# Optimization experiments

Hardware: AMD Instinct MI355X
Metric: run time of the kernel (lower is better)

The kernel has to match this reference:

```python
import jax, jax.numpy as jnp
import numpy as np
import math

B, C, N, M = 4, 128, 4096, 4096

def setup_inputs() -> dict:
    key = jax.random.key(0)
    ks = jax.random.split(key, 8)
    return {
        "x1": jax.random.normal(ks[0], (B, C, N), dtype=jnp.float32),
        "p1": jax.random.normal(ks[1], (B, 3, N), dtype=jnp.float32),
        "x2": jax.random.normal(ks[2], (B, C, M), dtype=jnp.float32),
        "p2": jax.random.normal(ks[3], (B, 3, M), dtype=jnp.float32),
        "Wq": jax.random.normal(ks[4], (C, C), dtype=jnp.float32) * 0.05,
        "Wk": jax.random.normal(ks[5], (C, C), dtype=jnp.float32) * 0.05,
        "Wv": jax.random.normal(ks[6], (C, C), dtype=jnp.float32) * 0.05,
        "Wpos": jax.random.normal(ks[7], (C, 3), dtype=jnp.float32) * 0.05,
    }

def reference(x1, p1, x2, p2, Wq, Wk, Wv, Wpos):
    # Conv1d with kernel_size=1, no bias == per-point matmul over channel dim.
    # NOTE: original forward uses self.pos for BOTH p1 and p2 (pos1 conv unused).
    pos = jnp.einsum('ck,bkn->bcn', Wpos, p1)   # [B,C,N]
    pos1 = jnp.einsum('ck,bkm->bcm', Wpos, p2)  # [B,C,M]
    q = jnp.einsum('dc,bcn->bdn', Wq, x1 + pos)   # [B,C,N]
    k = jnp.einsum('dc,bcm->bdm', Wk, x2 + pos1)  # [B,C,M]
    v = jnp.einsum('dc,bcm->bdm', Wv, x2)         # [B,C,M]
    scale = math.sqrt(q.shape[1])  # sqrt(C) -- q.shape[-2] in (B,C,N) layout
    energy = jnp.einsum('bcn,bcm->bnm', q, k) / scale  # [B,N,M]
    attention = jax.nn.softmax(energy, axis=-1)
    vout = jnp.einsum('bnm,bcm->bnc', attention, v)    # [B,N,C]
    out = jnp.swapaxes(vout, 1, 2) + x1                # [B,C,N] residual
    return jnp.swapaxes(out, 1, 2)                     # [B,N,C]
```

## Files before the change

kernel.cpp:

```cpp
#include <hip/hip_runtime.h>
#include <hip/hip_bf16.h>

#define B_ 4
#define C_ 128
#define N_ 4096
#define M_ 4096

typedef __bf16 bf16;
typedef __bf16 bf16x8 __attribute__((ext_vector_type(8)));
typedef float f32x4 __attribute__((ext_vector_type(4)));
typedef float f32x16 __attribute__((ext_vector_type(16)));

#define MFMA16(a, b, c) __builtin_amdgcn_mfma_f32_16x16x32_bf16(a, b, c, 0, 0, 0)
#define MFMA32(a, b, c) __builtin_amdgcn_mfma_f32_32x32x16_bf16(a, b, c, 0, 0, 0)

__device__ inline void gll16(const bf16* g, bf16* l) {
    __builtin_amdgcn_global_load_lds(
        (const __attribute__((address_space(1))) void*)g,
        (__attribute__((address_space(3))) void*)l, 16, 0, 0);
}

__device__ inline unsigned cvtpk(float a, float b) {
    unsigned r;
    asm("v_cvt_pk_bf16_f32 %0, %1, %2" : "=v"(r) : "v"(a), "v"(b));
    return r;
}

__global__ __launch_bounds__(256) void wcvt_kernel(
    const float* __restrict__ Wq, const float* __restrict__ Wk,
    const float* __restrict__ Wv, bf16* __restrict__ Wb) {
    int i = (blockIdx.x * 256 + threadIdx.x) * 4;
    const float* src = (i < 16384) ? Wq : (i < 32768) ? Wk : Wv;
    int off = i & 16383;
    float4 v = *(const float4*)(src + off);
    union { ushort4 u4; bf16 h[4]; } pk;
    pk.h[0] = (bf16)v.x; pk.h[1] = (bf16)v.y;
    pk.h[2] = (bf16)v.z; pk.h[3] = (bf16)v.w;
    *(ushort4*)(Wb + i) = pk.u4;
}

__global__ __launch_bounds__(512) void kvproj_kernel(
    const float* __restrict__ x2, const float* __restrict__ p2,
    const bf16* __restrict__ Wb, const float* __restrict__ Wpos,
    bf16* __restrict__ Kt, bf16* __restrict__ Vt) {
    __shared__ __align__(16) bf16 xp2[64 * 136];
    __shared__ __align__(16) bf16 xr2[64 * 136];
    __shared__ float pp[3 * 64], wls[384];

    const int t = threadIdx.x;
    const int b = blockIdx.y;
    const int n0 = blockIdx.x * 64;

    if (t < 48) {
        int k3 = t / 16, i4 = (t & 15) * 4;
        *(float4*)&pp[k3 * 64 + i4] =
            *(const float4*)(p2 + ((size_t)b * 3 + k3) * N_ + n0 + i4);
    } else if (t < 144) {
        int i4 = (t - 48) * 4;
        *(float4*)&wls[i4] = *(const float4*)(Wpos + i4);
    }
    __syncthreads();

    #pragma unroll
    for (int k = 0; k < 4; ++k) {
        int s = t + k * 512;
        int c = s >> 4, n4 = (s & 15) * 4;
        float4 xv = *(const float4*)(x2 + ((size_t)b * C_ + c) * N_ + n0 + n4);
        float w0 = wls[c * 3 + 0], w1 = wls[c * 3 + 1], w2 = wls[c * 3 + 2];
        const float* xa = &xv.x;
        #pragma unroll
        for (int j = 0; j < 4; ++j) {
            float pos = w0 * pp[n4 + j] + w1 * pp[64 + n4 + j] + w2 * pp[128 + n4 + j];
            xp2[(n4 + j) * 136 + c] = (bf16)(xa[j] + pos);
            xr2[(n4 + j) * 136 + c] = (bf16)xa[j];
        }
    }
    __syncthreads();

    const int w = t >> 6;
    const int lane = t & 63;
    const int col = lane & 15, quad = lane >> 4;
    const int band = w & 3;
    const int nl = band * 16 + col;
    const bool isK = (w < 4);

    const bf16* src = isK ? xp2 : xr2;
    const bf16* Wm = Wb + (isK ? 16384 : 32768);

    bf16x8 bx[4];
    #pragma unroll
    for (int cs = 0; cs < 4; ++cs)
        bx[cs] = *(const bf16x8*)&src[nl * 136 + cs * 32 + quad * 8];

    if (isK) {
        #pragma unroll
        for (int dt = 0; dt < 8; ++dt) {
            f32x4 acc = {0.f, 0.f, 0.f, 0.f};
            #pragma unroll
            for (int cs = 0; cs < 4; ++cs) {
                bf16x8 wf = *(const bf16x8*)(Wm + (dt * 16 + col) * 128 + cs * 32 + quad * 8);
                acc = MFMA16(bx[cs], wf, acc);
            }
            #pragma unroll
            for (int r = 0; r < 4; ++r) {
                int n = n0 + band * 16 + quad * 4 + r;
                Kt[((size_t)b * N_ + n) * C_ + dt * 16 + col] = (bf16)acc[r];
            }
        }
    } else {
        #pragma unroll
        for (int dt = 0; dt < 8; ++dt) {
            f32x4 acc = {0.f, 0.f, 0.f, 0.f};
            #pragma unroll
            for (int cs = 0; cs < 4; ++cs) {
                bf16x8 wf = *(const bf16x8*)(Wm + (dt * 16 + col) * 128 + cs * 32 + quad * 8);
                acc = MFMA16(wf, bx[cs], acc);
            }
            #pragma unroll
            for (int r = 0; r < 4; ++r)
                Vt[((size_t)b * C_ + dt * 16 + quad * 4 + r) * (size_t)M_ + n0 + nl] = (bf16)acc[r];
        }
    }
}

__global__ __launch_bounds__(512) void attn_kernel(
    const bf16* __restrict__ Kt, const bf16* __restrict__ Vt,
    const float* __restrict__ x1, const float* __restrict__ p1,
    const bf16* __restrict__ Wb, const float* __restrict__ Wpos,
    float* __restrict__ out) {
    __shared__ __align__(16) char smem[132096];

    const int t = threadIdx.x;
    const int w = t >> 6;
    const int lane = t & 63;
    const int col = lane & 31;
    const int hi = lane >> 5;
    const int kg = w & 3;
    const int qg = w >> 2;

    const int g0 = blockIdx.x;
    const int xcd = g0 & 7;
    const int b = xcd >> 1;
    const int qt = (xcd & 1) + ((g0 >> 3) << 1);
    const int n0 = qt * 64;

    const float KS = 0.12752107168406815f;

    const bf16* Kbase = Kt + (size_t)b * M_ * C_;
    const bf16* Vbase = Vt + (size_t)b * C_ * M_;

    bf16* xq = (bf16*)smem;
    float* ppq = (float*)(smem + 17408);
    float* wlsq = (float*)(smem + 18176);

    if (t < 48) {
        int k3 = t / 16, i4 = (t & 15) * 4;
        *(float4*)&ppq[k3 * 64 + i4] =
            *(const float4*)(p1 + ((size_t)b * 3 + k3) * N_ + n0 + i4);
    } else if (t < 144) {
        int i4 = (t - 48) * 4;
        *(float4*)&wlsq[i4] = *(const float4*)(Wpos + i4);
    }
    __syncthreads();

    #pragma unroll
    for (int k = 0; k < 4; ++k) {
        int s = t + k * 512;
        int c = s >> 4, n4 = (s & 15) * 4;
        float4 xv = *(const float4*)(x1 + ((size_t)b * C_ + c) * N_ + n0 + n4);
        float w0 = wlsq[c * 3 + 0], w1 = wlsq[c * 3 + 1], w2 = wlsq[c * 3 + 2];
        const float* xa = &xv.x;
        #pragma unroll
        for (int j = 0; j < 4; ++j) {
            float pos = w0 * ppq[n4 + j] + w1 * ppq[64 + n4 + j] + w2 * ppq[128 + n4 + j];
            xq[(n4 + j) * 136 + c] = (bf16)(xa[j] + pos);
        }
    }
    __syncthreads();

    {
        const int colq = lane & 15, quadq = lane >> 4;
        const int nlq = (w & 3) * 16 + colq;
        bf16x8 bxq[4];
        #pragma unroll
        for (int cs = 0; cs < 4; ++cs)
            bxq[cs] = *(const bf16x8*)&xq[nlq * 136 + cs * 32 + quadq * 8];
        __syncthreads();
        const int dt0 = (w >> 2) * 4;
        #pragma unroll
        for (int di = 0; di < 4; ++di) {
            int dt = dt0 + di;
            f32x4 acc = {0.f, 0.f, 0.f, 0.f};
            #pragma unroll
            for (int cs = 0; cs < 4; ++cs) {
                bf16x8 wf = *(const bf16x8*)(Wb + (dt * 16 + colq) * 128 + cs * 32 + quadq * 8);
                acc = MFMA16(bxq[cs], wf, acc);
            }
            #pragma unroll
            for (int r = 0; r < 4; ++r)
                xq[((w & 3) * 16 + quadq * 4 + r) * 136 + dt * 16 + colq] = (bf16)acc[r];
        }
        __syncthreads();
    }

    bf16x8 qf[8];
    #pragma unroll
    for (int cs = 0; cs < 8; ++cs)
        qf[cs] = *(const bf16x8*)&xq[(qg * 32 + col) * 136 + cs * 16 + hi * 8];
    asm volatile("s_waitcnt lgkmcnt(0)" ::: "memory");
    __builtin_amdgcn_sched_barrier(0);
    __builtin_amdgcn_s_barrier();

    f32x16 oacc[4];
    #pragma unroll
    for (int i = 0; i < 4; ++i)
        #pragma unroll
        for (int j = 0; j < 16; ++j) oacc[i][j] = 0.f;
    float lacc = 0.f;

    const int key_l = (kg << 5) + col;
    const int kxor = (key_l & 15) << 4;

    const bf16* kpp[4];
    const bf16* vpp[4];
    #pragma unroll
    for (int i = 0; i < 4; ++i) {
        int g = ((w << 2) + i) * 64 + lane;
        int row = g >> 4;
        int sp = (g & 15) ^ (row & 15);
        kpp[i] = Kbase + (size_t)row * C_ + sp * 8;
        vpp[i] = Vbase + (size_t)row * M_ + sp * 8;
    }

    auto stageK = [&](char* dst) {
        #pragma unroll
        for (int i = 0; i < 4; ++i) {
            gll16(kpp[i], (bf16*)dst + ((w << 2) + i) * 512);
            kpp[i] += 128 * C_;
        }
    };
    auto stageV = [&](char* dst) {
        #pragma unroll
        for (int i = 0; i < 4; ++i) {
            gll16(vpp[i], (bf16*)dst + ((w << 2) + i) * 512);
            vpp[i] += 128;
        }
    };

    stageK(smem);
    stageV(smem + 65536);
    stageK(smem + 32768);

    f32x16 sA0, sA1, sB0, sB1;

    auto qkc = [&](const char* kbBuf, f32x16& T0, f32x16& T1) {
        #pragma unroll
        for (int q = 0; q < 16; ++q) { T0[q] = 0.f; T1[q] = 0.f; }
        const char* kbp = kbBuf + key_l * 256;
        __builtin_amdgcn_s_setprio(1);
        #pragma unroll
        for (int cs = 0; cs < 4; ++cs) {
            bf16x8 kf = *(const bf16x8*)(kbp + ((((cs << 1) + hi) << 4) ^ kxor));
            T0 = MFMA32(kf, qf[cs], T0);
        }
        #pragma unroll
        for (int cs = 4; cs < 8; ++cs) {
            bf16x8 kf = *(const bf16x8*)(kbp + ((((cs << 1) + hi) << 4) ^ kxor));
            T1 = MFMA32(kf, qf[cs], T1);
        }
        __builtin_amdgcn_s_setprio(0);
    };

    auto smpv = [&](f32x16& S0, f32x16& S1, const char* vbBuf) {
        float p[16];
        #pragma unroll
        for (int r = 0; r < 16; ++r) {
            float e = fminf((S0[r] + S1[r]) * KS, 60.f);
            p[r] = __builtin_amdgcn_exp2f(e);
        }
        {
            float s01 = (p[0] + p[1]) + (p[2] + p[3]);
            float s23 = (p[4] + p[5]) + (p[6] + p[7]);
            float s45 = (p[8] + p[9]) + (p[10] + p[11]);
            float s67 = (p[12] + p[13]) + (p[14] + p[15]);
            lacc += (s01 + s23) + (s45 + s67);
        }
        unsigned W0 = cvtpk(p[0], p[1]),  W1 = cvtpk(p[2], p[3]);
        unsigned W2 = cvtpk(p[4], p[5]),  W3 = cvtpk(p[6], p[7]);
        unsigned W4 = cvtpk(p[8], p[9]),  W5 = cvtpk(p[10], p[11]);
        unsigned W6 = cvtpk(p[12], p[13]), W7 = cvtpk(p[14], p[15]);
        unsigned X0 = hi ? W0 : W2, X1 = hi ? W1 : W3;
        unsigned Y0 = hi ? W4 : W6, Y1 = hi ? W5 : W7;
        X0 = __shfl_xor(X0, 32, 64);  X1 = __shfl_xor(X1, 32, 64);
        Y0 = __shfl_xor(Y0, 32, 64);  Y1 = __shfl_xor(Y1, 32, 64);
        uint4 u0, u1;
        u0.x = hi ? X0 : W0;  u0.y = hi ? X1 : W1;
        u0.z = hi ? W2 : X0;  u0.w = hi ? W3 : X1;
        u1.x = hi ? Y0 : W4;  u1.y = hi ? Y1 : W5;
        u1.z = hi ? W6 : Y0;  u1.w = hi ? W7 : Y1;
        bf16x8 af0 = __builtin_bit_cast(bf16x8, u0);
        bf16x8 af1 = __builtin_bit_cast(bf16x8, u1);

        __builtin_amdgcn_s_setprio(1);
        #pragma unroll
        for (int ct = 0; ct < 4; ++ct) {
            int c = (ct << 5) + col;
            const char* vbp = vbBuf + c * 256;
            int vxor = (c & 15) << 4;
            bf16x8 vf0 = *(const bf16x8*)(vbp + ((((kg << 2) + hi) << 4) ^ vxor));
            bf16x8 vf1 = *(const bf16x8*)(vbp + ((((kg << 2) + 2 + hi) << 4) ^ vxor));
            oacc[ct] = MFMA32(af0, vf0, oacc[ct]);
            oacc[ct] = MFMA32(af1, vf1, oacc[ct]);
        }
        __builtin_amdgcn_s_setprio(0);
    };

    asm volatile("s_waitcnt vmcnt(8)" ::: "memory");
    __builtin_amdgcn_sched_barrier(0);
    __builtin_amdgcn_s_barrier();
    __builtin_amdgcn_sched_barrier(0);
    qkc(smem, sA0, sA1);

    for (int jp = 0; jp < 16; ++jp) {
        const int j0 = jp * 2, j1 = j0 + 1;

        asm volatile("s_waitcnt vmcnt(0)" ::: "memory");
        __builtin_amdgcn_sched_barrier(0);
        __builtin_amdgcn_s_barrier();
        __builtin_amdgcn_sched_barrier(0);
        if (j0 < 31) stageV(smem + 98304);
        if (j0 < 30) stageK(smem);
        if (j0 < 31) qkc(smem + 32768, sB0, sB1);
        smpv(sA0, sA1, smem + 65536);
        asm volatile("s_waitcnt lgkmcnt(0)" ::: "memory");
        __builtin_amdgcn_sched_barrier(0);

        asm volatile("s_waitcnt vmcnt(0)" ::: "memory");
        __builtin_amdgcn_sched_barrier(0);
        __builtin_amdgcn_s_barrier();
        __builtin_amdgcn_sched_barrier(0);
        if (j1 < 31) stageV(smem + 65536);
        if (j1 < 30) stageK(smem + 32768);
        if (j1 < 31) qkc(smem, sA0, sA1);
        smpv(sB0, sB1, smem + 98304);
        asm volatile("s_waitcnt lgkmcnt(0)" ::: "memory");
        __builtin_amdgcn_sched_barrier(0);
    }

    __builtin_amdgcn_s_barrier();

    float* obuf = (float*)smem;
    float* lps  = (float*)(smem + 131072);

    lacc += __shfl_xor(lacc, 32, 64);
    if (hi == 0) lps[(kg << 6) + (qg << 5) + col] = lacc;

    #pragma unroll
    for (int ct = 0; ct < 4; ++ct)
        #pragma unroll
        for (int r = 0; r < 16; ++r) {
            int q = (r & 3) + ((r >> 2) << 3) + (hi << 2);
            obuf[kg * 8192 + ((qg << 5) + q) * 128 + (ct << 5) + col] = oacc[ct][r];
        }
    __syncthreads();

    const int c2 = lane << 1;
    #pragma unroll
    for (int j = 0; j < 8; ++j) {
        int q = (w << 3) + j;
        float s0 = 0.f, s1 = 0.f;
        #pragma unroll
        for (int pp = 0; pp < 4; ++pp) {
            float2 v = *(const float2*)&obuf[pp * 8192 + q * 128 + c2];
            s0 += v.x; s1 += v.y;
        }
        float lsum = lps[q] + lps[64 + q] + lps[128 + q] + lps[192 + q];
        float linv = 1.0f / lsum;
        int n = n0 + q;
        float o0 = s0 * linv + x1[((size_t)b * C_ + c2) * N_ + n];
        float o1 = s1 * linv + x1[((size_t)b * C_ + c2 + 1) * N_ + n];
        *(float2*)&out[((size_t)b * N_ + n) * C_ + c2] = make_float2(o0, o1);
    }
}

extern "C" void kernel_launch(void* const* d_in, const int* in_sizes, int n_in,
                              void* d_out, int out_size, void* d_ws, size_t ws_size,
                              hipStream_t stream) {
    const float* x1   = (const float*)d_in[0];
    const float* p1   = (const float*)d_in[1];
    const float* x2   = (const float*)d_in[2];
    const float* p2   = (const float*)d_in[3];
    const float* Wq   = (const float*)d_in[4];
    const float* Wk   = (const float*)d_in[5];
    const float* Wv   = (const float*)d_in[6];
    const float* Wpos = (const float*)d_in[7];
    float* out = (float*)d_out;

    bf16* Wb = (bf16*)d_ws;
    bf16* Kt = Wb + 65536;
    bf16* Vt = Kt + (size_t)B_ * M_ * C_;

    wcvt_kernel<<<dim3(48), dim3(256), 0, stream>>>(Wq, Wk, Wv, Wb);
    kvproj_kernel<<<dim3(64, B_), dim3(512), 0, stream>>>(
        x2, p2, Wb, Wpos, Kt, Vt);
    attn_kernel<<<dim3(256), dim3(512), 0, stream>>>(
        Kt, Vt, x1, p1, Wb, Wpos, out);
}
```

Baseline: 144.3 us.

## Fuse weight conversion, KV projection and attention into one cooperative kernel

Merges the three launches (weight bf16 conversion, K/V projection, attention) into a single cooperative kernel of 256 blocks, using grid-wide syncs between phases. Each block converts a slice of the weights, projects its 64-point K/V tile (remapped so block index matches the attention tile mapping), then runs attention. This removes the launch overhead and inter-kernel gaps, at the cost of two grid barriers and the constraint that all blocks must be co-resident, with 512 threads and about 129KB LDS each.

After: 341.5 us. 137% more time.

```diff
diff --git a/kernel.cpp b/kernel.cpp
--- a/kernel.cpp
+++ b/kernel.cpp
@@ -1,5 +1,8 @@
 #include <hip/hip_runtime.h>
 #include <hip/hip_bf16.h>
+#include <hip/hip_cooperative_groups.h>
+
+namespace cg = cooperative_groups;
 
 #define B_ 4
 #define C_ 128
@@ -26,123 +29,123 @@
     return r;
 }
 
-__global__ __launch_bounds__(256) void wcvt_kernel(
+__global__ __launch_bounds__(512) void fused_kernel(
+    const float* __restrict__ x1, const float* __restrict__ p1,
+    const float* __restrict__ x2, const float* __restrict__ p2,
     const float* __restrict__ Wq, const float* __restrict__ Wk,
-    const float* __restrict__ Wv, bf16* __restrict__ Wb) {
-    int i = (blockIdx.x * 256 + threadIdx.x) * 4;
-    const float* src = (i < 16384) ? Wq : (i < 32768) ? Wk : Wv;
-    int off = i & 16383;
-    float4 v = *(const float4*)(src + off);
-    union { ushort4 u4; bf16 h[4]; } pk;
-    pk.h[0] = (bf16)v.x; pk.h[1] = (bf16)v.y;
-    pk.h[2] = (bf16)v.z; pk.h[3] = (bf16)v.w;
-    *(ushort4*)(Wb + i) = pk.u4;
-}
-
-__global__ __launch_bounds__(512) void kvproj_kernel(
-    const float* __restrict__ x2, const float* __restrict__ p2,
-    const bf16* __restrict__ Wb, const float* __restrict__ Wpos,
-    bf16* __restrict__ Kt, bf16* __restrict__ Vt) {
-    __shared__ __align__(16) bf16 xp2[64 * 136];
-    __shared__ __align__(16) bf16 xr2[64 * 136];
-    __shared__ float pp[3 * 64], wls[384];
-
-    const int t = threadIdx.x;
-    const int b = blockIdx.y;
-    const int n0 = blockIdx.x * 64;
-
-    if (t < 48) {
-        int k3 = t / 16, i4 = (t & 15) * 4;
-        *(float4*)&pp[k3 * 64 + i4] =
-            *(const float4*)(p2 + ((size_t)b * 3 + k3) * N_ + n0 + i4);
-    } else if (t < 144) {
-        int i4 = (t - 48) * 4;
-        *(float4*)&wls[i4] = *(const float4*)(Wpos + i4);
-    }
-    __syncthreads();
-
-    #pragma unroll
-    for (int k = 0; k < 4; ++k) {
-        int s = t + k * 512;
-        int c = s >> 4, n4 = (s & 15) * 4;
-        float4 xv = *(const float4*)(x2 + ((size_t)b * C_ + c) * N_ + n0 + n4);
-        float w0 = wls[c * 3 + 0], w1 = wls[c * 3 + 1], w2 = wls[c * 3 + 2];
-        const float* xa = &xv.x;
-        #pragma unroll
-        for (int j = 0; j < 4; ++j) {
-            float pos = w0 * pp[n4 + j] + w1 * pp[64 + n4 + j] + w2 * pp[128 + n4 + j];
-            xp2[(n4 + j) * 136 + c] = (bf16)(xa[j] + pos);
-            xr2[(n4 + j) * 136 + c] = (bf16)xa[j];
-        }
-    }
-    __syncthreads();
-
-    const int w = t >> 6;
-    const int lane = t & 63;
-    const int col = lane & 15, quad = lane >> 4;
-    const int band = w & 3;
-    const int nl = band * 16 + col;
-    const bool isK = (w < 4);
-
-    const bf16* src = isK ? xp2 : xr2;
-    const bf16* Wm = Wb + (isK ? 16384 : 32768);
-
-    bf16x8 bx[4];
-    #pragma unroll
-    for (int cs = 0; cs < 4; ++cs)
-        bx[cs] = *(const bf16x8*)&src[nl * 136 + cs * 32 + quad * 8];
-
-    if (isK) {
-        #pragma unroll
-        for (int dt = 0; dt < 8; ++dt) {
-            f32x4 acc = {0.f, 0.f, 0.f, 0.f};
-            #pragma unroll
-            for (int cs = 0; cs < 4; ++cs) {
-                bf16x8 wf = *(const bf16x8*)(Wm + (dt * 16 + col) * 128 + cs * 32 + quad * 8);
-                acc = MFMA16(bx[cs], wf, acc);
-            }
-            #pragma unroll
-            for (int r = 0; r < 4; ++r) {
-                int n = n0 + band * 16 + quad * 4 + r;
-                Kt[((size_t)b * N_ + n) * C_ + dt * 16 + col] = (bf16)acc[r];
-            }
-        }
-    } else {
-        #pragma unroll
-        for (int dt = 0; dt < 8; ++dt) {
-            f32x4 acc = {0.f, 0.f, 0.f, 0.f};
-            #pragma unroll
-            for (int cs = 0; cs < 4; ++cs) {
-                bf16x8 wf = *(const bf16x8*)(Wm + (dt * 16 + col) * 128 + cs * 32 + quad * 8);
-                acc = MFMA16(wf, bx[cs], acc);
-            }
-            #pragma unroll
-            for (int r = 0; r < 4; ++r)
-                Vt[((size_t)b * C_ + dt * 16 + quad * 4 + r) * (size_t)M_ + n0 + nl] = (bf16)acc[r];
-        }
-    }
-}
-
-__global__ __launch_bounds__(512) void attn_kernel(
-    const bf16* __restrict__ Kt, const bf16* __restrict__ Vt,
-    const float* __restrict__ x1, const float* __restrict__ p1,
-    const bf16* __restrict__ Wb, const float* __restrict__ Wpos,
+    const float* __restrict__ Wv, const float* __restrict__ Wpos,
+    bf16* __restrict__ Wb, bf16* __restrict__ Kt, bf16* __restrict__ Vt,
     float* __restrict__ out) {
     __shared__ __align__(16) char smem[132096];
+
+    cg::grid_group grid = cg::this_grid();
 
     const int t = threadIdx.x;
     const int w = t >> 6;
     const int lane = t & 63;
+    const int bid = blockIdx.x;
+
+    const int xcd = bid & 7;
+    const int b = xcd >> 1;
+    const int qt = (xcd & 1) + ((bid >> 3) << 1);
+    const int n0 = qt * 64;
+
+    if (t < 48) {
+        int i = bid * 192 + t * 4;
+        const float* src = (i < 16384) ? Wq : (i < 32768) ? Wk : Wv;
+        int off = i & 16383;
+        float4 v = *(const float4*)(src + off);
+        union { ushort4 u4; bf16 h[4]; } pk;
+        pk.h[0] = (bf16)v.x; pk.h[1] = (bf16)v.y;
+        pk.h[2] = (bf16)v.z; pk.h[3] = (bf16)v.w;
+        *(ushort4*)(Wb + i) = pk.u4;
+    }
+    __threadfence();
+    grid.sync();
+
+    {
+        bf16* xp2 = (bf16*)smem;
+        bf16* xr2 = (bf16*)(smem + 17408);
+        float* pp = (float*)(smem + 34816);
+        float* wls = (float*)(smem + 35584);
+
+        if (t < 48) {
+            int k3 = t / 16, i4 = (t & 15) * 4;
+            *(float4*)&pp[k3 * 64 + i4] =
+                *(const float4*)(p2 + ((size_t)b * 3 + k3) * N_ + n0 + i4);
+        } else if (t < 144) {
+            int i4 = (t - 48) * 4;
+            *(float4*)&wls[i4] = *(const float4*)(Wpos + i4);
+        }
+        __syncthreads();
+
+        #pragma unroll
+        for (int k = 0; k < 4; ++k) {
+            int s = t + k * 512;
+            int c = s >> 4, n4 = (s & 15) * 4;
+            float4 xv = *(const float4*)(x2 + ((size_t)b * C_ + c) * N_ + n0 + n4);
+            float w0 = wls[c * 3 + 0], w1 = wls[c * 3 + 1], w2 = wls[c * 3 + 2];
+            const float* xa = &xv.x;
+            #pragma unroll
+            for (int j = 0; j < 4; ++j) {
+                float pos = w0 * pp[n4 + j] + w1 * pp[64 + n4 + j] + w2 * pp[128 + n4 + j];
+                xp2[(n4 + j) * 136 + c] = (bf16)(xa[j] + pos);
+                xr2[(n4 + j) * 136 + c] = (bf16)xa[j];
+            }
+        }
+        __syncthreads();
+
+        const int colq = lane & 15, quadq = lane >> 4;
+        const int band = w & 3;
+        const int nl = band * 16 + colq;
+        const bool isK = (w < 4);
+
+        const bf16* src = isK ? xp2 : xr2;
+        const bf16* Wm = Wb + (isK ? 16384 : 32768);
+
+        bf16x8 bx[4];
+        #pragma unroll
+        for (int cs = 0; cs < 4; ++cs)
+            bx[cs] = *(const bf16x8*)&src[nl * 136 + cs * 32 + quadq * 8];
+
+        if (isK) {
+            #pragma unroll
+            for (int dt = 0; dt < 8; ++dt) {
+                f32x4 acc = {0.f, 0.f, 0.f, 0.f};
+                #pragma unroll
+                for (int cs = 0; cs < 4; ++cs) {
+                    bf16x8 wf = *(const bf16x8*)(Wm + (dt * 16 + colq) * 128 + cs * 32 + quadq * 8);
+                    acc = MFMA16(bx[cs], wf, acc);
+                }
+                #pragma unroll
+                for (int r = 0; r < 4; ++r) {
+                    int n = n0 + band * 16 + quadq * 4 + r;
+                    Kt[((size_t)b * N_ + n) * C_ + dt * 16 + colq] = (bf16)acc[r];
+                }
+            }
+        } else {
+            #pragma unroll
+            for (int dt = 0; dt < 8; ++dt) {
+                f32x4 acc = {0.f, 0.f, 0.f, 0.f};
+                #pragma unroll
+                for (int cs = 0; cs < 4; ++cs) {
+                    bf16x8 wf = *(const bf16x8*)(Wm + (dt * 16 + colq) * 128 + cs * 32 + quadq * 8);
+                    acc = MFMA16(wf, bx[cs], acc);
+                }
+                #pragma unroll
+                for (int r = 0; r < 4; ++r)
+                    Vt[((size_t)b * C_ + dt * 16 + quadq * 4 + r) * (size_t)M_ + n0 + nl] = (bf16)acc[r];
+            }
+        }
+    }
+    __threadfence();
+    grid.sync();
+    __threadfence();
+
     const int col = lane & 31;
     const int hi = lane >> 5;
     const int kg = w & 3;
     const int qg = w >> 2;
-
-    const int g0 = blockIdx.x;
-    const int xcd = g0 & 7;
-    const int b = xcd >> 1;
-    const int qt = (xcd & 1) + ((g0 >> 3) << 1);
-    const int n0 = qt * 64;
 
     const float KS = 0.12752107168406815f;
 
@@ -370,8 +373,8 @@
         int q = (w << 3) + j;
         float s0 = 0.f, s1 = 0.f;
         #pragma unroll
-        for (int pp = 0; pp < 4; ++pp) {
-            float2 v = *(const float2*)&obuf[pp * 8192 + q * 128 + c2];
+        for (int pp2_ = 0; pp2_ < 4; ++pp2_) {
+            float2 v = *(const float2*)&obuf[pp2_ * 8192 + q * 128 + c2];
             s0 += v.x; s1 += v.y;
         }
         float lsum = lps[q] + lps[64 + q] + lps[128 + q] + lps[192 + q];
@@ -398,11 +401,13 @@
 
     bf16* Wb = (bf16*)d_ws;
     bf16* Kt = Wb + 65536;
-    bf16* Vt = Kt + (size_t)B_ * M_ * C_;
-
-    wcvt_kernel<<<dim3(48), dim3(256), 0, stream>>>(Wq, Wk, Wv, Wb);
-    kvproj_kernel<<<dim3(64, B_), dim3(512), 0, stream>>>(
-        x2, p2, Wb, Wpos, Kt, Vt);
-    attn_kernel<<<dim3(256), dim3(512), 0, stream>>>(
-        Kt, Vt, x1, p1, Wb, Wpos, out);
+    bf16* Vt = Kt + (size_t)B_ * N_ * C_;
+
+    void* args[] = {
+        (void*)&x1, (void*)&p1, (void*)&x2, (void*)&p2,
+        (void*)&Wq, (void*)&Wk, (void*)&Wv, (void*)&Wpos,
+        (void*)&Wb, (void*)&Kt, (void*)&Vt, (void*)&out
+    };
+    hipLaunchCooperativeKernel((const void*)fused_kernel,
+                               dim3(256), dim3(512), args, 0, stream);
 }
```

## Shrink attention blocks to 4 waves with 64-key chunks and simple double buffer

Applied to the files above, without the earlier changes.

The attention kernel now runs 256 threads per block with 2 key groups instead of 4, processes 64-key chunks instead of 128, and halves shared memory so two blocks can fit per CU. The two-stage software pipeline that overlapped QK of one chunk with softmax·V of the previous is replaced by a plain double-buffered loop that does QK, softmax and PV on the same chunk. This trades intra-block overlap for more resident blocks and adds twice as many barriers per key sweep. The V tile swizzle is adjusted to 8-segment rows.

Result: slower. 170.4 us (+18.1%).

```diff
diff --git a/kernel.cpp b/kernel.cpp
--- a/kernel.cpp
+++ b/kernel.cpp
@@ -123,20 +123,20 @@
     }
 }
 
-__global__ __launch_bounds__(512) void attn_kernel(
+__global__ __launch_bounds__(256) void attn_kernel(
     const bf16* __restrict__ Kt, const bf16* __restrict__ Vt,
     const float* __restrict__ x1, const float* __restrict__ p1,
     const bf16* __restrict__ Wb, const float* __restrict__ Wpos,
     float* __restrict__ out) {
-    __shared__ __align__(16) char smem[132096];
+    __shared__ __align__(16) char smem[66048];
 
     const int t = threadIdx.x;
     const int w = t >> 6;
     const int lane = t & 63;
     const int col = lane & 31;
     const int hi = lane >> 5;
-    const int kg = w & 3;
-    const int qg = w >> 2;
+    const int kg = w & 1;
+    const int qg = w >> 1;
 
     const int g0 = blockIdx.x;
     const int xcd = g0 & 7;
@@ -164,8 +164,8 @@
     __syncthreads();
 
     #pragma unroll
-    for (int k = 0; k < 4; ++k) {
-        int s = t + k * 512;
+    for (int k = 0; k < 8; ++k) {
+        int s = t + k * 256;
         int c = s >> 4, n4 = (s & 15) * 4;
         float4 xv = *(const float4*)(x1 + ((size_t)b * C_ + c) * N_ + n0 + n4);
         float w0 = wlsq[c * 3 + 0], w1 = wlsq[c * 3 + 1], w2 = wlsq[c * 3 + 2];
@@ -180,16 +180,14 @@
 
     {
         const int colq = lane & 15, quadq = lane >> 4;
-        const int nlq = (w & 3) * 16 + colq;
+        const int nlq = w * 16 + colq;
         bf16x8 bxq[4];
         #pragma unroll
         for (int cs = 0; cs < 4; ++cs)
             bxq[cs] = *(const bf16x8*)&xq[nlq * 136 + cs * 32 + quadq * 8];
         __syncthreads();
-        const int dt0 = (w >> 2) * 4;
-        #pragma unroll
-        for (int di = 0; di < 4; ++di) {
-            int dt = dt0 + di;
+        #pragma unroll
+        for (int dt = 0; dt < 8; ++dt) {
             f32x4 acc = {0.f, 0.f, 0.f, 0.f};
             #pragma unroll
             for (int cs = 0; cs < 4; ++cs) {
@@ -198,7 +196,7 @@
             }
             #pragma unroll
             for (int r = 0; r < 4; ++r)
-                xq[((w & 3) * 16 + quadq * 4 + r) * 136 + dt * 16 + colq] = (bf16)acc[r];
+                xq[(w * 16 + quadq * 4 + r) * 136 + dt * 16 + colq] = (bf16)acc[r];
         }
         __syncthreads();
     }
@@ -226,56 +224,66 @@
     #pragma unroll
     for (int i = 0; i < 4; ++i) {
         int g = ((w << 2) + i) * 64 + lane;
-        int row = g >> 4;
-        int sp = (g & 15) ^ (row & 15);
-        kpp[i] = Kbase + (size_t)row * C_ + sp * 8;
-        vpp[i] = Vbase + (size_t)row * M_ + sp * 8;
+        int krow = g >> 4;
+        int ksp = (g & 15) ^ (krow & 15);
+        kpp[i] = Kbase + (size_t)krow * C_ + ksp * 8;
+        int vrow = g >> 3;
+        int vsp = (g & 7) ^ (vrow & 7);
+        vpp[i] = Vbase + (size_t)vrow * M_ + vsp * 8;
     }
 
     auto stageK = [&](char* dst) {
         #pragma unroll
         for (int i = 0; i < 4; ++i) {
             gll16(kpp[i], (bf16*)dst + ((w << 2) + i) * 512);
-            kpp[i] += 128 * C_;
+            kpp[i] += 64 * C_;
         }
     };
     auto stageV = [&](char* dst) {
         #pragma unroll
         for (int i = 0; i < 4; ++i) {
             gll16(vpp[i], (bf16*)dst + ((w << 2) + i) * 512);
-            vpp[i] += 128;
+            vpp[i] += 64;
         }
     };
 
     stageK(smem);
-    stageV(smem + 65536);
-    stageK(smem + 32768);
-
-    f32x16 sA0, sA1, sB0, sB1;
-
-    auto qkc = [&](const char* kbBuf, f32x16& T0, f32x16& T1) {
-        #pragma unroll
-        for (int q = 0; q < 16; ++q) { T0[q] = 0.f; T1[q] = 0.f; }
-        const char* kbp = kbBuf + key_l * 256;
+    stageV(smem + 32768);
+
+    int buf = 0;
+    for (int ch = 0; ch < 64; ++ch) {
+        asm volatile("s_waitcnt vmcnt(0)" ::: "memory");
+        __builtin_amdgcn_sched_barrier(0);
+        __builtin_amdgcn_s_barrier();
+        __builtin_amdgcn_sched_barrier(0);
+
+        if (ch < 63) {
+            stageK(smem + ((buf ^ 1) << 14));
+            stageV(smem + 32768 + ((buf ^ 1) << 14));
+        }
+
+        const char* kbp = smem + (buf << 14) + key_l * 256;
+
+        f32x16 s0a, s1a;
+        #pragma unroll
+        for (int j = 0; j < 16; ++j) { s0a[j] = 0.f; s1a[j] = 0.f; }
         __builtin_amdgcn_s_setprio(1);
         #pragma unroll
         for (int cs = 0; cs < 4; ++cs) {
             bf16x8 kf = *(const bf16x8*)(kbp + ((((cs << 1) + hi) << 4) ^ kxor));
-            T0 = MFMA32(kf, qf[cs], T0);
+            s0a = MFMA32(kf, qf[cs], s0a);
         }
         #pragma unroll
         for (int cs = 4; cs < 8; ++cs) {
             bf16x8 kf = *(const bf16x8*)(kbp + ((((cs << 1) + hi) << 4) ^ kxor));
-            T1 = MFMA32(kf, qf[cs], T1);
+            s1a = MFMA32(kf, qf[cs], s1a);
         }
         __builtin_amdgcn_s_setprio(0);
-    };
-
-    auto smpv = [&](f32x16& S0, f32x16& S1, const char* vbBuf) {
+
         float p[16];
         #pragma unroll
         for (int r = 0; r < 16; ++r) {
-            float e = fminf((S0[r] + S1[r]) * KS, 60.f);
+            float e = fminf((s0a[r] + s1a[r]) * KS, 60.f);
             p[r] = __builtin_amdgcn_exp2f(e);
         }
         {
@@ -301,56 +309,29 @@
         bf16x8 af0 = __builtin_bit_cast(bf16x8, u0);
         bf16x8 af1 = __builtin_bit_cast(bf16x8, u1);
 
+        const char* vbB = smem + 32768 + (buf << 14);
         __builtin_amdgcn_s_setprio(1);
         #pragma unroll
         for (int ct = 0; ct < 4; ++ct) {
             int c = (ct << 5) + col;
-            const char* vbp = vbBuf + c * 256;
-            int vxor = (c & 15) << 4;
+            const char* vbp = vbB + c * 128;
+            int vxor = (c & 7) << 4;
             bf16x8 vf0 = *(const bf16x8*)(vbp + ((((kg << 2) + hi) << 4) ^ vxor));
             bf16x8 vf1 = *(const bf16x8*)(vbp + ((((kg << 2) + 2 + hi) << 4) ^ vxor));
             oacc[ct] = MFMA32(af0, vf0, oacc[ct]);
             oacc[ct] = MFMA32(af1, vf1, oacc[ct]);
         }
         __builtin_amdgcn_s_setprio(0);
-    };
-
-    asm volatile("s_waitcnt vmcnt(8)" ::: "memory");
-    __builtin_amdgcn_sched_barrier(0);
-    __builtin_amdgcn_s_barrier();
-    __builtin_amdgcn_sched_barrier(0);
-    qkc(smem, sA0, sA1);
-
-    for (int jp = 0; jp < 16; ++jp) {
-        const int j0 = jp * 2, j1 = j0 + 1;
-
-        asm volatile("s_waitcnt vmcnt(0)" ::: "memory");
-        __builtin_amdgcn_sched_barrier(0);
-        __builtin_amdgcn_s_barrier();
-        __builtin_amdgcn_sched_barrier(0);
-        if (j0 < 31) stageV(smem + 98304);
-        if (j0 < 30) stageK(smem);
-        if (j0 < 31) qkc(smem + 32768, sB0, sB1);
-        smpv(sA0, sA1, smem + 65536);
+
         asm volatile("s_waitcnt lgkmcnt(0)" ::: "memory");
         __builtin_amdgcn_sched_barrier(0);
-
-        asm volatile("s_waitcnt vmcnt(0)" ::: "memory");
-        __builtin_amdgcn_sched_barrier(0);
-        __builtin_amdgcn_s_barrier();
-        __builtin_amdgcn_sched_barrier(0);
-        if (j1 < 31) stageV(smem + 65536);
-        if (j1 < 30) stageK(smem + 32768);
-        if (j1 < 31) qkc(smem, sA0, sA1);
-        smpv(sB0, sB1, smem + 98304);
-        asm volatile("s_waitcnt lgkmcnt(0)" ::: "memory");
-        __builtin_amdgcn_sched_barrier(0);
+        buf ^= 1;
     }
 
     __builtin_amdgcn_s_barrier();
 
     float* obuf = (float*)smem;
-    float* lps  = (float*)(smem + 131072);
+    float* lps  = (float*)(smem + 65536);
 
     lacc += __shfl_xor(lacc, 32, 64);
     if (hi == 0) lps[(kg << 6) + (qg << 5) + col] = lacc;
@@ -366,15 +347,12 @@
 
     const int c2 = lane << 1;
     #pragma unroll
-    for (int j = 0; j < 8; ++j) {
-        int q = (w << 3) + j;
-        float s0 = 0.f, s1 = 0.f;
-        #pragma unroll
-        for (int pp = 0; pp < 4; ++pp) {
-            float2 v = *(const float2*)&obuf[pp * 8192 + q * 128 + c2];
-            s0 += v.x; s1 += v.y;
-        }
-        float lsum = lps[q] + lps[64 + q] + lps[128 + q] + lps[192 + q];
+    for (int j = 0; j < 16; ++j) {
+        int q = (w << 4) + j;
+        float2 v0 = *(const float2*)&obuf[q * 128 + c2];
+        float2 v1 = *(const float2*)&obuf[8192 + q * 128 + c2];
+        float s0 = v0.x + v1.x, s1 = v0.y + v1.y;
+        float lsum = lps[q] + lps[64 + q];
         float linv = 1.0f / lsum;
         int n = n0 + q;
         float o0 = s0 * linv + x1[((size_t)b * C_ + c2) * N_ + n];
@@ -398,11 +376,11 @@
 
     bf16* Wb = (bf16*)d_ws;
     bf16* Kt = Wb + 65536;
-    bf16* Vt = Kt + (size_t)B_ * M_ * C_;
+    bf16* Vt = Kt + (size_t)B_ * N_ * C_;
 
     wcvt_kernel<<<dim3(48), dim3(256), 0, stream>>>(Wq, Wk, Wv, Wb);
     kvproj_kernel<<<dim3(64, B_), dim3(512), 0, stream>>>(
         x2, p2, Wb, Wpos, Kt, Vt);
-    attn_kernel<<<dim3(256), dim3(512), 0, stream>>>(
+    attn_kernel<<<dim3(256), dim3(256), 0, stream>>>(
         Kt, Vt, x1, p1, Wb, Wpos, out);
 }
```

## Fold softmax scale into Wq and restructure attention loop into single-stage double buffer

Applied to the files above, without the earlier changes.

Folds the softmax scale factor into the bf16 Wq conversion, which removes the per-element multiply in the softmax. It replaces the software-pipelined QK/PV schedule, where the next tile's QK ran while the current tile's PV ran, with a simpler double-buffered body. Each step stages K and V together, then does QK and PV on the same tile. LDS addresses are precomputed as constant offsets, the QK accumulation uses one chain instead of two, and the cross-half lane shuffles are replaced with permlane32_swap when the compiler supports it. This lowers register pressure and per-iteration instruction count, but loses the overlap of QK with PV from adjacent tiles, and the single accumulation chain lengthens the MFMA dependency.

Result: faster. 140.9 us (-2.4%).

```diff
diff --git a/kernel.cpp b/kernel.cpp
--- a/kernel.cpp
+++ b/kernel.cpp
@@ -10,6 +10,7 @@
 typedef __bf16 bf16x8 __attribute__((ext_vector_type(8)));
 typedef float f32x4 __attribute__((ext_vector_type(4)));
 typedef float f32x16 __attribute__((ext_vector_type(16)));
+typedef unsigned u32x2 __attribute__((ext_vector_type(2)));
 
 #define MFMA16(a, b, c) __builtin_amdgcn_mfma_f32_16x16x32_bf16(a, b, c, 0, 0, 0)
 #define MFMA32(a, b, c) __builtin_amdgcn_mfma_f32_32x32x16_bf16(a, b, c, 0, 0, 0)
@@ -31,11 +32,12 @@
     const float* __restrict__ Wv, bf16* __restrict__ Wb) {
     int i = (blockIdx.x * 256 + threadIdx.x) * 4;
     const float* src = (i < 16384) ? Wq : (i < 32768) ? Wk : Wv;
+    float scale = (i < 16384) ? 0.12752107168406815f : 1.0f;
     int off = i & 16383;
     float4 v = *(const float4*)(src + off);
     union { ushort4 u4; bf16 h[4]; } pk;
-    pk.h[0] = (bf16)v.x; pk.h[1] = (bf16)v.y;
-    pk.h[2] = (bf16)v.z; pk.h[3] = (bf16)v.w;
+    pk.h[0] = (bf16)(v.x * scale); pk.h[1] = (bf16)(v.y * scale);
+    pk.h[2] = (bf16)(v.z * scale); pk.h[3] = (bf16)(v.w * scale);
     *(ushort4*)(Wb + i) = pk.u4;
 }
 
@@ -144,8 +146,6 @@
     const int qt = (xcd & 1) + ((g0 >> 3) << 1);
     const int n0 = qt * 64;
 
-    const float KS = 0.12752107168406815f;
-
     const bf16* Kbase = Kt + (size_t)b * M_ * C_;
     const bf16* Vbase = Vt + (size_t)b * C_ * M_;
 
@@ -216,68 +216,65 @@
     for (int i = 0; i < 4; ++i)
         #pragma unroll
         for (int j = 0; j < 16; ++j) oacc[i][j] = 0.f;
+    f32x16 Z;
+    #pragma unroll
+    for (int j = 0; j < 16; ++j) Z[j] = 0.f;
     float lacc = 0.f;
 
     const int key_l = (kg << 5) + col;
     const int kxor = (key_l & 15) << 4;
 
-    const bf16* kpp[4];
-    const bf16* vpp[4];
+    int kaddr[8];
+    #pragma unroll
+    for (int cs = 0; cs < 8; ++cs)
+        kaddr[cs] = key_l * 256 + (((((cs << 1) + hi)) << 4) ^ kxor);
+    const int vaddrA = 65536 + col * 256 + (((((kg << 2) + hi)) << 4) ^ ((col & 15) << 4));
+    const int vaddrB = vaddrA ^ 32;
+
+    const bf16* Kchunk = Kbase;
+    const bf16* Vchunk = Vbase;
+    int koff[4], voff[4];
     #pragma unroll
     for (int i = 0; i < 4; ++i) {
         int g = ((w << 2) + i) * 64 + lane;
         int row = g >> 4;
         int sp = (g & 15) ^ (row & 15);
-        kpp[i] = Kbase + (size_t)row * C_ + sp * 8;
-        vpp[i] = Vbase + (size_t)row * M_ + sp * 8;
-    }
-
-    auto stageK = [&](char* dst) {
-        #pragma unroll
-        for (int i = 0; i < 4; ++i) {
-            gll16(kpp[i], (bf16*)dst + ((w << 2) + i) * 512);
-            kpp[i] += 128 * C_;
-        }
+        koff[i] = row * C_ + sp * 8;
+        voff[i] = row * M_ + sp * 8;
+    }
+
+    auto stage = [&](int kbDst, int vbDst) {
+        #pragma unroll
+        for (int i = 0; i < 4; ++i)
+            gll16(Kchunk + koff[i], (bf16*)(smem + kbDst) + ((w << 2) + i) * 512);
+        #pragma unroll
+        for (int i = 0; i < 4; ++i)
+            gll16(Vchunk + voff[i], (bf16*)(smem + vbDst) + ((w << 2) + i) * 512);
+        Kchunk += 128 * C_;
+        Vchunk += 128;
     };
-    auto stageV = [&](char* dst) {
-        #pragma unroll
-        for (int i = 0; i < 4; ++i) {
-            gll16(vpp[i], (bf16*)dst + ((w << 2) + i) * 512);
-            vpp[i] += 128;
-        }
-    };
-
-    stageK(smem);
-    stageV(smem + 65536);
-    stageK(smem + 32768);
-
-    f32x16 sA0, sA1, sB0, sB1;
-
-    auto qkc = [&](const char* kbBuf, f32x16& T0, f32x16& T1) {
-        #pragma unroll
-        for (int q = 0; q < 16; ++q) { T0[q] = 0.f; T1[q] = 0.f; }
-        const char* kbp = kbBuf + key_l * 256;
+
+    auto body = [&](int kbImm, int vbImm, int kbDst, int vbDst, bool doStage) {
+        asm volatile("s_waitcnt vmcnt(0)" ::: "memory");
+        __builtin_amdgcn_sched_barrier(0);
+        __builtin_amdgcn_s_barrier();
+        __builtin_amdgcn_sched_barrier(0);
+        if (doStage) stage(kbDst, vbDst);
+
         __builtin_amdgcn_s_setprio(1);
-        #pragma unroll
-        for (int cs = 0; cs < 4; ++cs) {
-            bf16x8 kf = *(const bf16x8*)(kbp + ((((cs << 1) + hi) << 4) ^ kxor));
-            T0 = MFMA32(kf, qf[cs], T0);
-        }
-        #pragma unroll
-        for (int cs = 4; cs < 8; ++cs) {
-            bf16x8 kf = *(const bf16x8*)(kbp + ((((cs << 1) + hi) << 4) ^ kxor));
-            T1 = MFMA32(kf, qf[cs], T1);
+        bf16x8 kf0 = *(const bf16x8*)(smem + kbImm + kaddr[0]);
+        f32x16 sacc = MFMA32(kf0, qf[0], Z);
+        #pragma unroll
+        for (int cs = 1; cs < 8; ++cs) {
+            bf16x8 kf = *(const bf16x8*)(smem + kbImm + kaddr[cs]);
+            sacc = MFMA32(kf, qf[cs], sacc);
         }
         __builtin_amdgcn_s_setprio(0);
-    };
-
-    auto smpv = [&](f32x16& S0, f32x16& S1, const char* vbBuf) {
+
         float p[16];
         #pragma unroll
-        for (int r = 0; r < 16; ++r) {
-            float e = fminf((S0[r] + S1[r]) * KS, 60.f);
-            p[r] = __builtin_amdgcn_exp2f(e);
-        }
+        for (int r = 0; r < 16; ++r)
+            p[r] = __builtin_amdgcn_exp2f(fminf(sacc[r], 60.f));
         {
             float s01 = (p[0] + p[1]) + (p[2] + p[3]);
             float s23 = (p[4] + p[5]) + (p[6] + p[7]);
@@ -289,62 +286,48 @@
         unsigned W2 = cvtpk(p[4], p[5]),  W3 = cvtpk(p[6], p[7]);
         unsigned W4 = cvtpk(p[8], p[9]),  W5 = cvtpk(p[10], p[11]);
         unsigned W6 = cvtpk(p[12], p[13]), W7 = cvtpk(p[14], p[15]);
+        uint4 u0, u1;
+#if __has_builtin(__builtin_amdgcn_permlane32_swap)
+        u32x2 r0 = __builtin_amdgcn_permlane32_swap(W0, W2, false, false);
+        u0.x = r0[0]; u0.z = r0[1];
+        u32x2 r1 = __builtin_amdgcn_permlane32_swap(W1, W3, false, false);
+        u0.y = r1[0]; u0.w = r1[1];
+        u32x2 r2 = __builtin_amdgcn_permlane32_swap(W4, W6, false, false);
+        u1.x = r2[0]; u1.z = r2[1];
+        u32x2 r3 = __builtin_amdgcn_permlane32_swap(W5, W7, false, false);
+        u1.y = r3[0]; u1.w = r3[1];
+#else
         unsigned X0 = hi ? W0 : W2, X1 = hi ? W1 : W3;
         unsigned Y0 = hi ? W4 : W6, Y1 = hi ? W5 : W7;
         X0 = __shfl_xor(X0, 32, 64);  X1 = __shfl_xor(X1, 32, 64);
         Y0 = __shfl_xor(Y0, 32, 64);  Y1 = __shfl_xor(Y1, 32, 64);
-        uint4 u0, u1;
         u0.x = hi ? X0 : W0;  u0.y = hi ? X1 : W1;
         u0.z = hi ? W2 : X0;  u0.w = hi ? W3 : X1;
         u1.x = hi ? Y0 : W4;  u1.y = hi ? Y1 : W5;
         u1.z = hi ? W6 : Y0;  u1.w = hi ? W7 : Y1;
+#endif
         bf16x8 af0 = __builtin_bit_cast(bf16x8, u0);
         bf16x8 af1 = __builtin_bit_cast(bf16x8, u1);
 
         __builtin_amdgcn_s_setprio(1);
         #pragma unroll
         for (int ct = 0; ct < 4; ++ct) {
-            int c = (ct << 5) + col;
-            const char* vbp = vbBuf + c * 256;
-            int vxor = (c & 15) << 4;
-            bf16x8 vf0 = *(const bf16x8*)(vbp + ((((kg << 2) + hi) << 4) ^ vxor));
-            bf16x8 vf1 = *(const bf16x8*)(vbp + ((((kg << 2) + 2 + hi) << 4) ^ vxor));
+            bf16x8 vf0 = *(const bf16x8*)(smem + vbImm + ct * 8192 + vaddrA);
+            bf16x8 vf1 = *(const bf16x8*)(smem + vbImm + ct * 8192 + vaddrB);
             oacc[ct] = MFMA32(af0, vf0, oacc[ct]);
             oacc[ct] = MFMA32(af1, vf1, oacc[ct]);
         }
         __builtin_amdgcn_s_setprio(0);
-    };
-
-    asm volatile("s_waitcnt vmcnt(8)" ::: "memory");
-    __builtin_amdgcn_sched_barrier(0);
-    __builtin_amdgcn_s_barrier();
-    __builtin_amdgcn_sched_barrier(0);
-    qkc(smem, sA0, sA1);
-
-    for (int jp = 0; jp < 16; ++jp) {
-        const int j0 = jp * 2, j1 = j0 + 1;
-
-        asm volatile("s_waitcnt vmcnt(0)" ::: "memory");
-        __builtin_amdgcn_sched_barrier(0);
-        __builtin_amdgcn_s_barrier();
-        __builtin_amdgcn_sched_barrier(0);
-        if (j0 < 31) stageV(smem + 98304);
-        if (j0 < 30) stageK(smem);
-        if (j0 < 31) qkc(smem + 32768, sB0, sB1);
-        smpv(sA0, sA1, smem + 65536);
+
         asm volatile("s_waitcnt lgkmcnt(0)" ::: "memory");
         __builtin_amdgcn_sched_barrier(0);
-
-        asm volatile("s_waitcnt vmcnt(0)" ::: "memory");
-        __builtin_amdgcn_sched_barrier(0);
-        __builtin_amdgcn_s_barrier();
-        __builtin_amdgcn_sched_barrier(0);
-        if (j1 < 31) stageV(smem + 65536);
-        if (j1 < 30) stageK(smem + 32768);
-        if (j1 < 31) qkc(smem, sA0, sA1);
-        smpv(sB0, sB1, smem + 98304);
-        asm volatile("s_waitcnt lgkmcnt(0)" ::: "memory");
-        __builtin_amdgcn_sched_barrier(0);
+    };
+
+    stage(0, 65536);
+    #pragma unroll 1
+    for (int jp = 0; jp < 16; ++jp) {
+        body(0, 0, 32768, 98304, true);
+        body(32768, 32768, 0, 65536, jp < 15);
     }
 
     __builtin_amdgcn_s_barrier();
@@ -370,8 +353,8 @@
         int q = (w << 3) + j;
         float s0 = 0.f, s1 = 0.f;
         #pragma unroll
-        for (int pp = 0; pp < 4; ++pp) {
-            float2 v = *(const float2*)&obuf[pp * 8192 + q * 128 + c2];
+        for (int pp2_ = 0; pp2_ < 4; ++pp2_) {
+            float2 v = *(const float2*)&obuf[pp2_ * 8192 + q * 128 + c2];
             s0 += v.x; s1 += v.y;
         }
         float lsum = lps[q] + lps[64 + q] + lps[128 + q] + lps[192 + q];
@@ -398,7 +381,7 @@
 
     bf16* Wb = (bf16*)d_ws;
     bf16* Kt = Wb + 65536;
-    bf16* Vt = Kt + (size_t)B_ * M_ * C_;
+    bf16* Vt = Kt + (size_t)B_ * N_ * C_;
 
     wcvt_kernel<<<dim3(48), dim3(256), 0, stream>>>(Wq, Wk, Wv, Wb);
     kvproj_kernel<<<dim3(64, B_), dim3(512), 0, stream>>>(
```
